# Kernel tuning notes

Measured on AMD Instinct MI355X. Metric: run time of the kernel, lower is better.

The kernel has to match this reference:

```python
import jax, jax.numpy as jnp
import numpy as np

GAMMA = 0.5
BATCH, DIM, UNITS = 16384, 512, 1024


def setup_inputs() -> dict:
    key = jax.random.key(0)
    k1, k2 = jax.random.split(key)
    inputs = jax.random.normal(k1, (BATCH, DIM), dtype=jnp.float32)
    mu = jax.random.normal(k2, (DIM, UNITS), dtype=jnp.float32)
    return {"inputs": inputs, "mu": mu}


def reference(inputs, mu):
    # Squared L2 distance from each input row to each center (column of mu):
    x_sq = jnp.sum(inputs * inputs, axis=1, keepdims=True)        # [B, 1]
    mu_sq = jnp.sum(mu * mu, axis=0, keepdims=True)               # [1, U]
    cross = inputs @ mu                                           # [B, U] GEMM
    l2 = x_sq - 2.0 * cross + mu_sq                                # [B, U]
    return jnp.exp(-GAMMA * l2)
```

## Files before the change

### kernel.cpp

```cpp
#include <hip/hip_runtime.h>
#include <hip/hip_bf16.h>

#define BATCH 16384
#define DIM   512
#define UNITS 1024
#define GAMMA 0.5f

typedef __bf16 v8bf __attribute__((ext_vector_type(8)));
typedef __bf16 v4bf __attribute__((ext_vector_type(4)));
typedef float  v4f  __attribute__((ext_vector_type(4)));

__device__ __forceinline__ void async_copy16(const void* g, void* l) {
    __builtin_amdgcn_global_load_lds(
        (const __attribute__((address_space(1))) void*)g,
        (__attribute__((address_space(3))) void*)l,
        16 , 0 , 0 );
}

__global__ void prep_a_kernel(const float* __restrict__ in,
                              __bf16* __restrict__ A,
                              float* __restrict__ xsq) {
    const int row = blockIdx.x;
    const int t   = threadIdx.x;
    float4 v = ((const float4*)(in + (size_t)row * DIM))[t];
    float s = v.x * v.x + v.y * v.y + v.z * v.z + v.w * v.w;
    v4bf b;
    b[0] = (__bf16)v.x; b[1] = (__bf16)v.y; b[2] = (__bf16)v.z; b[3] = (__bf16)v.w;
    ((v4bf*)A)[(size_t)row * (DIM / 4) + t] = b;
    for (int off = 32; off; off >>= 1) s += __shfl_down(s, off, 64);
    __shared__ float red[2];
    if ((t & 63) == 0) red[t >> 6] = s;
    __syncthreads();
    if (t == 0) xsq[row] = red[0] + red[1];
}

__global__ void prep_b_kernel(const float* __restrict__ mu,
                              __bf16* __restrict__ Bt,
                              float* __restrict__ musq) {
    const int n = blockIdx.x;
    const int t = threadIdx.x;
    float s = 0.f;
    for (int k = t; k < DIM; k += 128) {
        float v = mu[(size_t)k * UNITS + n];
        s += v * v;
        Bt[(size_t)n * DIM + k] = (__bf16)v;
    }
    for (int off = 32; off; off >>= 1) s += __shfl_down(s, off, 64);
    __shared__ float red[2];
    if ((t & 63) == 0) red[t >> 6] = s;
    __syncthreads();
    if (t == 0) musq[n] = red[0] + red[1];
}

__global__ __launch_bounds__(256)
void rbf_gemm_kernel(const __bf16* __restrict__ A,
                     const __bf16* __restrict__ Bt,
                     const float* __restrict__ xsq,
                     const float* __restrict__ musq,
                     float* __restrict__ out) {
    __shared__ __attribute__((aligned(16))) __bf16 As[128 * 32];
    __shared__ __attribute__((aligned(16))) __bf16 Bs[128 * 32];

    const int t    = threadIdx.x;
    const int lane = t & 63;
    const int wave = t >> 6;
    const int quad = lane >> 4;
    const int lr   = lane & 15;
    const int wm   = (wave >> 1) * 64;
    const int wn   = (wave & 1) * 64;
    const int m0   = blockIdx.x * 128;
    const int n0   = blockIdx.y * 128;

    v4f acc[4][4];
#pragma unroll
    for (int i = 0; i < 4; i++)
#pragma unroll
        for (int j = 0; j < 4; j++) acc[i][j] = (v4f)0.f;

    const int fr = t >> 2;
    const int fc = (t & 3) * 8;
    const __bf16* ga0 = A  + (size_t)(m0 + fr)      * DIM + fc;
    const __bf16* ga1 = A  + (size_t)(m0 + 64 + fr) * DIM + fc;
    const __bf16* gb0 = Bt + (size_t)(n0 + fr)      * DIM + fc;
    const __bf16* gb1 = Bt + (size_t)(n0 + 64 + fr) * DIM + fc;
    __bf16* la0 = As + wave * 512;
    __bf16* la1 = As + 2048 + wave * 512;
    __bf16* lb0 = Bs + wave * 512;
    __bf16* lb1 = Bs + 2048 + wave * 512;

    for (int kt = 0; kt < DIM / 32; kt++) {
        const int k0 = kt * 32;
        async_copy16(ga0 + k0, la0);
        async_copy16(ga1 + k0, la1);
        async_copy16(gb0 + k0, lb0);
        async_copy16(gb1 + k0, lb1);
        __syncthreads();

        v8bf af[4], bfr[4];
#pragma unroll
        for (int i = 0; i < 4; i++)
            af[i] = *(const v8bf*)(As + (wm + i * 16 + lr) * 32 + quad * 8);
#pragma unroll
        for (int j = 0; j < 4; j++)
            bfr[j] = *(const v8bf*)(Bs + (wn + j * 16 + lr) * 32 + quad * 8);
#pragma unroll
        for (int i = 0; i < 4; i++)
#pragma unroll
            for (int j = 0; j < 4; j++)
                acc[i][j] = __builtin_amdgcn_mfma_f32_16x16x32_bf16(
                    af[i], bfr[j], acc[i][j], 0, 0, 0);
        __syncthreads();
    }

    float mq[4];
#pragma unroll
    for (int j = 0; j < 4; j++) mq[j] = musq[n0 + wn + j * 16 + lr];

#pragma unroll
    for (int i = 0; i < 4; i++) {
#pragma unroll
        for (int r = 0; r < 4; r++) {
            const int grow = m0 + wm + i * 16 + quad * 4 + r;
            const float xs = xsq[grow];
            float* orow = out + (size_t)grow * UNITS + n0 + wn + lr;
#pragma unroll
            for (int j = 0; j < 4; j++) {
                float l2 = xs - 2.0f * acc[i][j][r] + mq[j];
                orow[j * 16] = __expf(-GAMMA * l2);
            }
        }
    }
}

extern "C" void kernel_launch(void* const* d_in, const int* in_sizes, int n_in,
                              void* d_out, int out_size, void* d_ws, size_t ws_size,
                              hipStream_t stream) {
    const float* inputs = (const float*)d_in[0];
    const float* mu     = (const float*)d_in[1];
    float* out = (float*)d_out;

    char* ws = (char*)d_ws;
    __bf16* A    = (__bf16*)ws;
    __bf16* Bt   = (__bf16*)(ws + (size_t)BATCH * DIM * 2);
    float*  xsq  = (float*)(ws + (size_t)BATCH * DIM * 2 + (size_t)UNITS * DIM * 2);
    float*  musq = xsq + BATCH;

    prep_a_kernel<<<BATCH, 128, 0, stream>>>(inputs, A, xsq);
    prep_b_kernel<<<UNITS, 128, 0, stream>>>(mu, Bt, musq);
    rbf_gemm_kernel<<<dim3(BATCH / 128, UNITS / 128), 256, 0, stream>>>(
        A, Bt, xsq, musq, out);
}
```

Measured before the change: 122.4 us.

## Widen GEMM K-tile to 64 with XOR-swizzled LDS and rework prep kernels

The GEMM now stages 64-wide K tiles per barrier pair instead of 32, halving the number of sync rounds, and applies an XOR swizzle to the async global-to-LDS copies and the fragment reads to avoid LDS bank conflicts. prep_a processes four rows per block with one wave per row, using a wave-only reduction and 16-byte stores. prep_b replaces strided column reads of mu with a 64x64 LDS-tiled transpose so global loads coalesce and the Bt stores are vectorized. The cost is doubled LDS per GEMM block, which may lower occupancy.

```diff
diff --git a/kernel.cpp b/kernel.cpp
--- a/kernel.cpp
+++ b/kernel.cpp
@@ -7,7 +7,6 @@
 #define GAMMA 0.5f
 
 typedef __bf16 v8bf __attribute__((ext_vector_type(8)));
-typedef __bf16 v4bf __attribute__((ext_vector_type(4)));
 typedef float  v4f  __attribute__((ext_vector_type(4)));
 
 __device__ __forceinline__ void async_copy16(const void* g, void* l) {
@@ -17,39 +16,66 @@
         16 , 0 , 0 );
 }
 
-__global__ void prep_a_kernel(const float* __restrict__ in,
-                              __bf16* __restrict__ A,
-                              float* __restrict__ xsq) {
-    const int row = blockIdx.x;
-    const int t   = threadIdx.x;
-    float4 v = ((const float4*)(in + (size_t)row * DIM))[t];
-    float s = v.x * v.x + v.y * v.y + v.z * v.z + v.w * v.w;
-    v4bf b;
-    b[0] = (__bf16)v.x; b[1] = (__bf16)v.y; b[2] = (__bf16)v.z; b[3] = (__bf16)v.w;
-    ((v4bf*)A)[(size_t)row * (DIM / 4) + t] = b;
+__global__ __launch_bounds__(256)
+void prep_a_kernel(const float* __restrict__ in,
+                   __bf16* __restrict__ A,
+                   float* __restrict__ xsq) {
+    const int t    = threadIdx.x;
+    const int lane = t & 63;
+    const int row  = blockIdx.x * 4 + (t >> 6);
+    const float4* src = (const float4*)(in + (size_t)row * DIM);
+    float4 a = src[lane * 2];
+    float4 b = src[lane * 2 + 1];
+    float s = a.x * a.x + a.y * a.y + a.z * a.z + a.w * a.w
+            + b.x * b.x + b.y * b.y + b.z * b.z + b.w * b.w;
+    v8bf o;
+    o[0] = (__bf16)a.x; o[1] = (__bf16)a.y; o[2] = (__bf16)a.z; o[3] = (__bf16)a.w;
+    o[4] = (__bf16)b.x; o[5] = (__bf16)b.y; o[6] = (__bf16)b.z; o[7] = (__bf16)b.w;
+    *(v8bf*)(A + (size_t)row * DIM + lane * 8) = o;
     for (int off = 32; off; off >>= 1) s += __shfl_down(s, off, 64);
-    __shared__ float red[2];
-    if ((t & 63) == 0) red[t >> 6] = s;
-    __syncthreads();
-    if (t == 0) xsq[row] = red[0] + red[1];
+    if (lane == 0) xsq[row] = s;
 }
 
-__global__ void prep_b_kernel(const float* __restrict__ mu,
-                              __bf16* __restrict__ Bt,
-                              float* __restrict__ musq) {
-    const int n = blockIdx.x;
-    const int t = threadIdx.x;
+__global__ __launch_bounds__(256)
+void prep_b_kernel(const float* __restrict__ mu,
+                   __bf16* __restrict__ Bt,
+                   float* __restrict__ musq) {
+    __shared__ float lds[64][65];
+    __shared__ float red[64][4];
+    const int t  = threadIdx.x;
+    const int n0 = blockIdx.x * 64;
+    const int c  = t & 63;
+    const int r4 = t >> 6;
+    const int nl = t >> 2;
+    const int ks = (t & 3) * 16;
     float s = 0.f;
-    for (int k = t; k < DIM; k += 128) {
-        float v = mu[(size_t)k * UNITS + n];
-        s += v * v;
-        Bt[(size_t)n * DIM + k] = (__bf16)v;
+    for (int kc = 0; kc < DIM; kc += 64) {
+        __syncthreads();
+#pragma unroll
+        for (int i = 0; i < 16; i++) {
+            const int k = r4 + i * 4;
+            lds[k][c] = mu[(size_t)(kc + k) * UNITS + n0 + c];
+        }
+        __syncthreads();
+        v8bf o0, o1;
+#pragma unroll
+        for (int j = 0; j < 8; j++) {
+            float v = lds[ks + j][nl];
+            s += v * v;
+            o0[j] = (__bf16)v;
+        }
+#pragma unroll
+        for (int j = 0; j < 8; j++) {
+            float v = lds[ks + 8 + j][nl];
+            s += v * v;
+            o1[j] = (__bf16)v;
+        }
+        *(v8bf*)(Bt + (size_t)(n0 + nl) * DIM + kc + ks) = o0;
+        *(v8bf*)(Bt + (size_t)(n0 + nl) * DIM + kc + ks + 8) = o1;
     }
-    for (int off = 32; off; off >>= 1) s += __shfl_down(s, off, 64);
-    __shared__ float red[2];
-    if ((t & 63) == 0) red[t >> 6] = s;
+    red[nl][t & 3] = s;
     __syncthreads();
-    if (t == 0) musq[n] = red[0] + red[1];
+    if (t < 64) musq[n0 + t] = red[t][0] + red[t][1] + red[t][2] + red[t][3];
 }
 
 __global__ __launch_bounds__(256)
@@ -58,8 +84,8 @@
                      const float* __restrict__ xsq,
                      const float* __restrict__ musq,
                      float* __restrict__ out) {
-    __shared__ __attribute__((aligned(16))) __bf16 As[128 * 32];
-    __shared__ __attribute__((aligned(16))) __bf16 Bs[128 * 32];
+    __shared__ __attribute__((aligned(16))) __bf16 As[128 * 64];
+    __shared__ __attribute__((aligned(16))) __bf16 Bs[128 * 64];
 
     const int t    = threadIdx.x;
     const int lane = t & 63;
@@ -77,38 +103,53 @@
 #pragma unroll
         for (int j = 0; j < 4; j++) acc[i][j] = (v4f)0.f;
 
-    const int fr = t >> 2;
-    const int fc = (t & 3) * 8;
-    const __bf16* ga0 = A  + (size_t)(m0 + fr)      * DIM + fc;
-    const __bf16* ga1 = A  + (size_t)(m0 + 64 + fr) * DIM + fc;
-    const __bf16* gb0 = Bt + (size_t)(n0 + fr)      * DIM + fc;
-    const __bf16* gb1 = Bt + (size_t)(n0 + 64 + fr) * DIM + fc;
-    __bf16* la0 = As + wave * 512;
-    __bf16* la1 = As + 2048 + wave * 512;
-    __bf16* lb0 = Bs + wave * 512;
-    __bf16* lb1 = Bs + 2048 + wave * 512;
+    const int fr_base = t >> 3;
+    const int swz     = (t & 7) ^ (fr_base & 7);
+    const __bf16* ga[4];
+    const __bf16* gb[4];
+#pragma unroll
+    for (int it = 0; it < 4; it++) {
+        ga[it] = A  + (size_t)(m0 + it * 32 + fr_base) * DIM + swz * 8;
+        gb[it] = Bt + (size_t)(n0 + it * 32 + fr_base) * DIM + swz * 8;
+    }
+    __bf16* la[4];
+    __bf16* lb[4];
+#pragma unroll
+    for (int it = 0; it < 4; it++) {
+        la[it] = As + it * 2048 + wave * 512;
+        lb[it] = Bs + it * 2048 + wave * 512;
+    }
 
-    for (int kt = 0; kt < DIM / 32; kt++) {
-        const int k0 = kt * 32;
-        async_copy16(ga0 + k0, la0);
-        async_copy16(ga1 + k0, la1);
-        async_copy16(gb0 + k0, lb0);
-        async_copy16(gb1 + k0, lb1);
+    const int sL = quad ^ (lr & 7);
+    const int arow = (wm + lr) * 64;
+    const int brow = (wn + lr) * 64;
+
+    for (int kt = 0; kt < DIM / 64; kt++) {
+        const int k0 = kt * 64;
+#pragma unroll
+        for (int it = 0; it < 4; it++) {
+            async_copy16(ga[it] + k0, la[it]);
+            async_copy16(gb[it] + k0, lb[it]);
+        }
         __syncthreads();
 
-        v8bf af[4], bfr[4];
 #pragma unroll
-        for (int i = 0; i < 4; i++)
-            af[i] = *(const v8bf*)(As + (wm + i * 16 + lr) * 32 + quad * 8);
+        for (int kh = 0; kh < 2; kh++) {
+            const int so = (sL ^ (kh << 2)) * 8;
+            v8bf af[4], bfr[4];
 #pragma unroll
-        for (int j = 0; j < 4; j++)
-            bfr[j] = *(const v8bf*)(Bs + (wn + j * 16 + lr) * 32 + quad * 8);
-#pragma unroll
-        for (int i = 0; i < 4; i++)
+            for (int i = 0; i < 4; i++)
+                af[i] = *(const v8bf*)(As + arow + i * 1024 + so);
 #pragma unroll
             for (int j = 0; j < 4; j++)
-                acc[i][j] = __builtin_amdgcn_mfma_f32_16x16x32_bf16(
-                    af[i], bfr[j], acc[i][j], 0, 0, 0);
+                bfr[j] = *(const v8bf*)(Bs + brow + j * 1024 + so);
+#pragma unroll
+            for (int i = 0; i < 4; i++)
+#pragma unroll
+                for (int j = 0; j < 4; j++)
+                    acc[i][j] = __builtin_amdgcn_mfma_f32_16x16x32_bf16(
+                        af[i], bfr[j], acc[i][j], 0, 0, 0);
+        }
         __syncthreads();
     }
 
@@ -145,8 +186,8 @@
     float*  xsq  = (float*)(ws + (size_t)BATCH * DIM * 2 + (size_t)UNITS * DIM * 2);
     float*  musq = xsq + BATCH;
 
-    prep_a_kernel<<<BATCH, 128, 0, stream>>>(inputs, A, xsq);
-    prep_b_kernel<<<UNITS, 128, 0, stream>>>(mu, Bt, musq);
+    prep_a_kernel<<<BATCH / 4, 256, 0, stream>>>(inputs, A, xsq);
+    prep_b_kernel<<<UNITS / 64, 256, 0, stream>>>(mu, Bt, musq);
     rbf_gemm_kernel<<<dim3(BATCH / 128, UNITS / 128), 256, 0, stream>>>(
         A, Bt, xsq, musq, out);
 }
```

Measured after the change: 121.0 us. Within noise of the previous version (-1.2%).

## Switch GEMM to fp8 MFMA with fused A conversion and larger tiles

Applied to the files above, without the earlier changes.

Replaces the bf16 pipeline with fp8: mu is transposed through LDS and packed to fp8 once, while input rows are read as fp32 directly in the GEMM, converted to fp8 in registers, and squared-summed in place, which removes the separate A-prep kernel and its workspace round trip. The GEMM now uses 32x32x16 fp8 MFMA on 256x256 tiles with a swizzled LDS layout for B and only two K stages. The aim is to cut prep traffic and double matrix throughput. In exchange it loses considerable precision, since fp8 e4m3 for the cross term inside an exponential can break tolerance, and A is loaded uncoalesced without LDS staging.

```diff
diff --git a/kernel.cpp b/kernel.cpp
--- a/kernel.cpp
+++ b/kernel.cpp
@@ -4,11 +4,8 @@
 #define BATCH 16384
 #define DIM   512
 #define UNITS 1024
-#define GAMMA 0.5f
 
-typedef __bf16 v8bf __attribute__((ext_vector_type(8)));
-typedef __bf16 v4bf __attribute__((ext_vector_type(4)));
-typedef float  v4f  __attribute__((ext_vector_type(4)));
+typedef float v16f __attribute__((ext_vector_type(16)));
 
 __device__ __forceinline__ void async_copy16(const void* g, void* l) {
     __builtin_amdgcn_global_load_lds(
@@ -17,117 +14,119 @@
         16 , 0 , 0 );
 }
 
-__global__ void prep_a_kernel(const float* __restrict__ in,
-                              __bf16* __restrict__ A,
-                              float* __restrict__ xsq) {
-    const int row = blockIdx.x;
-    const int t   = threadIdx.x;
-    float4 v = ((const float4*)(in + (size_t)row * DIM))[t];
-    float s = v.x * v.x + v.y * v.y + v.z * v.z + v.w * v.w;
-    v4bf b;
-    b[0] = (__bf16)v.x; b[1] = (__bf16)v.y; b[2] = (__bf16)v.z; b[3] = (__bf16)v.w;
-    ((v4bf*)A)[(size_t)row * (DIM / 4) + t] = b;
-    for (int off = 32; off; off >>= 1) s += __shfl_down(s, off, 64);
-    __shared__ float red[2];
-    if ((t & 63) == 0) red[t >> 6] = s;
+__global__ __launch_bounds__(256)
+void prep_b_kernel(const float* __restrict__ mu, unsigned char* __restrict__ Bt,
+                   float* __restrict__ musq) {
+    __shared__ float lds[64][65];
+    __shared__ float red[64][4];
+    const int t  = threadIdx.x;
+    const int n0 = blockIdx.x * 64;
+    const int c  = t & 63, r4 = t >> 6;
+    const int nl = t >> 2, kp = t & 3;
+    float s = 0.f;
+    for (int kc = 0; kc < DIM; kc += 64) {
+        __syncthreads();
+#pragma unroll
+        for (int i = 0; i < 16; i++)
+            lds[r4 + i * 4][c] = mu[(size_t)(kc + r4 + i * 4) * UNITS + n0 + c];
+        __syncthreads();
+        int wr[4];
+#pragma unroll
+        for (int q = 0; q < 4; q++) {
+            float f0 = lds[kp * 16 + q * 4 + 0][nl];
+            float f1 = lds[kp * 16 + q * 4 + 1][nl];
+            float f2 = lds[kp * 16 + q * 4 + 2][nl];
+            float f3 = lds[kp * 16 + q * 4 + 3][nl];
+            s += f0 * f0 + f1 * f1 + f2 * f2 + f3 * f3;
+            int v = __builtin_amdgcn_cvt_pk_fp8_f32(f0, f1, 0, false);
+            wr[q]  = __builtin_amdgcn_cvt_pk_fp8_f32(f2, f3, v, true);
+        }
+        *(int4*)(Bt + (size_t)(n0 + nl) * DIM + kc + kp * 16) =
+            make_int4(wr[0], wr[1], wr[2], wr[3]);
+    }
+    red[nl][kp] = s;
     __syncthreads();
-    if (t == 0) xsq[row] = red[0] + red[1];
+    if (t < 64) musq[n0 + t] = red[t][0] + red[t][1] + red[t][2] + red[t][3];
 }
 
-__global__ void prep_b_kernel(const float* __restrict__ mu,
-                              __bf16* __restrict__ Bt,
-                              float* __restrict__ musq) {
-    const int n = blockIdx.x;
-    const int t = threadIdx.x;
-    float s = 0.f;
-    for (int k = t; k < DIM; k += 128) {
-        float v = mu[(size_t)k * UNITS + n];
-        s += v * v;
-        Bt[(size_t)n * DIM + k] = (__bf16)v;
-    }
-    for (int off = 32; off; off >>= 1) s += __shfl_down(s, off, 64);
-    __shared__ float red[2];
-    if ((t & 63) == 0) red[t >> 6] = s;
-    __syncthreads();
-    if (t == 0) musq[n] = red[0] + red[1];
-}
-
-__global__ __launch_bounds__(256)
-void rbf_gemm_kernel(const __bf16* __restrict__ A,
-                     const __bf16* __restrict__ Bt,
-                     const float* __restrict__ xsq,
+__global__ __launch_bounds__(512, 2)
+void rbf_gemm_kernel(const float* __restrict__ A,
+                     const unsigned char* __restrict__ Bt,
                      const float* __restrict__ musq,
                      float* __restrict__ out) {
-    __shared__ __attribute__((aligned(16))) __bf16 As[128 * 32];
-    __shared__ __attribute__((aligned(16))) __bf16 Bs[128 * 32];
+    __shared__ __attribute__((aligned(16))) unsigned char Bs[256 * 256];
 
-    const int t    = threadIdx.x;
-    const int lane = t & 63;
-    const int wave = t >> 6;
-    const int quad = lane >> 4;
-    const int lr   = lane & 15;
-    const int wm   = (wave >> 1) * 64;
-    const int wn   = (wave & 1) * 64;
-    const int m0   = blockIdx.x * 128;
-    const int n0   = blockIdx.y * 128;
+    const int t  = threadIdx.x;
+    const int l  = t & 63;
+    const int w  = t >> 6;
+    const int h  = l >> 5;
+    const int ln = l & 31;
+    const int m0 = blockIdx.x * 256;
+    const int n0 = blockIdx.y * 256;
+    const int sx = l & 15;
 
-    v4f acc[4][4];
+    const int arow = m0 + w * 32 + ln;
+    const float* Ap = A + (size_t)arow * DIM;
+
+    v16f acc[8];
 #pragma unroll
-    for (int i = 0; i < 4; i++)
+    for (int j = 0; j < 8; j++) acc[j] = (v16f)0.f;
+    float xq = 0.f;
+
+    for (int half = 0; half < 2; half++) {
+        const int kc = half * 256;
+        __syncthreads();
 #pragma unroll
-        for (int j = 0; j < 4; j++) acc[i][j] = (v4f)0.f;
-
-    const int fr = t >> 2;
-    const int fc = (t & 3) * 8;
-    const __bf16* ga0 = A  + (size_t)(m0 + fr)      * DIM + fc;
-    const __bf16* ga1 = A  + (size_t)(m0 + 64 + fr) * DIM + fc;
-    const __bf16* gb0 = Bt + (size_t)(n0 + fr)      * DIM + fc;
-    const __bf16* gb1 = Bt + (size_t)(n0 + 64 + fr) * DIM + fc;
-    __bf16* la0 = As + wave * 512;
-    __bf16* la1 = As + 2048 + wave * 512;
-    __bf16* lb0 = Bs + wave * 512;
-    __bf16* lb1 = Bs + 2048 + wave * 512;
-
-    for (int kt = 0; kt < DIM / 32; kt++) {
-        const int k0 = kt * 32;
-        async_copy16(ga0 + k0, la0);
-        async_copy16(ga1 + k0, la1);
-        async_copy16(gb0 + k0, lb0);
-        async_copy16(gb1 + k0, lb1);
+        for (int i = 0; i < 8; i++) {
+            const int C  = i * 512 + t;
+            const int n  = C >> 4;
+            const int sl = (C & 15) ^ (n & 15);
+            async_copy16(Bt + (size_t)(n0 + n) * DIM + kc + sl * 16,
+                         Bs + C * 16);
+        }
         __syncthreads();
 
-        v8bf af[4], bfr[4];
+        const float* ap = Ap + kc + h * 8;
+        const unsigned char* bbase = Bs + ln * 256 + h * 8;
 #pragma unroll
-        for (int i = 0; i < 4; i++)
-            af[i] = *(const v8bf*)(As + (wm + i * 16 + lr) * 32 + quad * 8);
+        for (int s = 0; s < 16; s++) {
+            float4 f0 = *(const float4*)(ap);
+            float4 f1 = *(const float4*)(ap + 4);
+            ap += 16;
+            xq += f0.x * f0.x + f0.y * f0.y + f0.z * f0.z + f0.w * f0.w
+                + f1.x * f1.x + f1.y * f1.y + f1.z * f1.z + f1.w * f1.w;
+            int alo = __builtin_amdgcn_cvt_pk_fp8_f32(f0.x, f0.y, 0, false);
+            alo     = __builtin_amdgcn_cvt_pk_fp8_f32(f0.z, f0.w, alo, true);
+            int ahi = __builtin_amdgcn_cvt_pk_fp8_f32(f1.x, f1.y, 0, false);
+            ahi     = __builtin_amdgcn_cvt_pk_fp8_f32(f1.z, f1.w, ahi, true);
+            long a8 = ((long)(unsigned)ahi << 32) | (unsigned)alo;
+            const unsigned char* bp = bbase + (s ^ sx) * 16;
 #pragma unroll
-        for (int j = 0; j < 4; j++)
-            bfr[j] = *(const v8bf*)(Bs + (wn + j * 16 + lr) * 32 + quad * 8);
-#pragma unroll
-        for (int i = 0; i < 4; i++)
-#pragma unroll
-            for (int j = 0; j < 4; j++)
-                acc[i][j] = __builtin_amdgcn_mfma_f32_16x16x32_bf16(
-                    af[i], bfr[j], acc[i][j], 0, 0, 0);
-        __syncthreads();
+            for (int j = 0; j < 8; j++) {
+                long b8 = *(const long*)(bp + j * 8192);
+                acc[j] = __builtin_amdgcn_mfma_f32_32x32x16_fp8_fp8(
+                    a8, b8, acc[j], 0, 0, 0);
+            }
+        }
     }
 
-    float mq[4];
+    float xs = xq + __shfl_xor(xq, 32, 64);
+
+    float mb[8];
 #pragma unroll
-    for (int j = 0; j < 4; j++) mq[j] = musq[n0 + wn + j * 16 + lr];
+    for (int j = 0; j < 8; j++) mb[j] = -0.5f * musq[n0 + j * 32 + ln];
 
 #pragma unroll
-    for (int i = 0; i < 4; i++) {
+    for (int rq = 0; rq < 4; rq++) {
 #pragma unroll
-        for (int r = 0; r < 4; r++) {
-            const int grow = m0 + wm + i * 16 + quad * 4 + r;
-            const float xs = xsq[grow];
-            float* orow = out + (size_t)grow * UNITS + n0 + wn + lr;
+        for (int rr = 0; rr < 4; rr++) {
+            const int r    = rq * 4 + rr;
+            const int rowp = rr + 8 * rq + 4 * h;
+            const float xb = -0.5f * __shfl(xs, rowp, 64);
+            float* orow = out + (size_t)(m0 + w * 32 + rowp) * UNITS + n0 + ln;
 #pragma unroll
-            for (int j = 0; j < 4; j++) {
-                float l2 = xs - 2.0f * acc[i][j][r] + mq[j];
-                orow[j * 16] = __expf(-GAMMA * l2);
-            }
+            for (int j = 0; j < 8; j++)
+                orow[j * 32] = __expf(acc[j][r] + xb + mb[j]);
         }
     }
 }
@@ -140,13 +139,10 @@
     float* out = (float*)d_out;
 
     char* ws = (char*)d_ws;
-    __bf16* A    = (__bf16*)ws;
-    __bf16* Bt   = (__bf16*)(ws + (size_t)BATCH * DIM * 2);
-    float*  xsq  = (float*)(ws + (size_t)BATCH * DIM * 2 + (size_t)UNITS * DIM * 2);
-    float*  musq = xsq + BATCH;
+    unsigned char* Bt = (unsigned char*)ws;
+    float* musq       = (float*)(ws + (size_t)UNITS * DIM);
 
-    prep_a_kernel<<<BATCH, 128, 0, stream>>>(inputs, A, xsq);
-    prep_b_kernel<<<UNITS, 128, 0, stream>>>(mu, Bt, musq);
-    rbf_gemm_kernel<<<dim3(BATCH / 128, UNITS / 128), 256, 0, stream>>>(
-        A, Bt, xsq, musq, out);
+    prep_b_kernel<<<UNITS / 64, 256, 0, stream>>>(mu, Bt, musq);
+    rbf_gemm_kernel<<<dim3(BATCH / 256, UNITS / 256), 512, 0, stream>>>(
+        inputs, Bt, musq, out);
 }
```

After: 121.6 us. About the same (-0.7%).
